# Optimization experiments

Hardware: AMD Instinct MI355X
Metric: run time of the kernel (lower is better)

The kernel has to match this reference:

```python
import jax, jax.numpy as jnp
import numpy as np

B, S, D = 2, 2048, 768
H = 12
HD = D // H  # 64
SCALE = HD ** -0.5


def setup_inputs() -> dict:
    key = jax.random.key(0)
    k1, k2, k3, k4, k5 = jax.random.split(key, 5)
    x = jax.random.normal(k1, (B, S, D), dtype=jnp.float32)
    w_qkv = jax.random.normal(k2, (D, 3 * D), dtype=jnp.float32) * (D ** -0.5)
    b_qkv = jax.random.normal(k3, (3 * D,), dtype=jnp.float32) * 0.02
    w_proj = jax.random.normal(k4, (D, D), dtype=jnp.float32) * (D ** -0.5)
    b_proj = jax.random.normal(k5, (D,), dtype=jnp.float32) * 0.02
    return {"x": x, "w_qkv": w_qkv, "b_qkv": b_qkv, "w_proj": w_proj, "b_proj": b_proj}


def reference(x, w_qkv, b_qkv, w_proj, b_proj):
    b, s, d = x.shape
    # QKV projection: (B,S,3D) -> (3,B,H,S,HD)
    qkv = x @ w_qkv + b_qkv
    qkv = qkv.reshape(b, s, 3, H, HD).transpose(2, 0, 3, 1, 4)
    q, k, v = qkv[0], qkv[1], qkv[2]
    q = q * SCALE
    # full NxN attention scores, as in the original module
    attn = jnp.einsum("bhqd,bhkd->bhqk", q, k)
    attn = jax.nn.softmax(attn, axis=-1)
    out = jnp.einsum("bhqk,bhkd->bhqd", attn, v)  # (B,H,S,HD)
    out = out.transpose(0, 2, 1, 3).reshape(b, s, d)
    return out @ w_proj + b_proj
```

## Files before the change

kernel.cpp:

```cpp
#include <hip/hip_runtime.h>
#include <hip/hip_bf16.h>

#define B_ 2
#define S_ 2048
#define D_ 768
#define H_ 12
#define HD_ 64
#define EXP2C_ 0.1803368801111244f

typedef __attribute__((ext_vector_type(8))) short bf16x8;
typedef __attribute__((ext_vector_type(8))) unsigned short u16x8;
typedef __attribute__((ext_vector_type(4))) float f32x4;

static __device__ __forceinline__ unsigned short f2bf(float x) {
    union { float f; unsigned u; } v; v.f = x;
    unsigned r = (v.u + 0x7FFFu + ((v.u >> 16) & 1u)) >> 16;
    return (unsigned short)r;
}
static __device__ __forceinline__ float bf2f(unsigned short h) {
    union { unsigned u; float f; } v; v.u = ((unsigned)h) << 16;
    return v.f;
}
static __device__ __forceinline__ float fexp2(float x) { return __builtin_exp2f(x); }

static __device__ __forceinline__ unsigned pk_bf16(float a, float b) {
    __hip_bfloat162 pk = __float22bfloat162_rn(make_float2(a, b));
    union { __hip_bfloat162 h; unsigned u; } v; v.h = pk;
    return v.u;
}

static __device__ __forceinline__ f32x4 mfma32(bf16x8 a, bf16x8 b, f32x4 c) {
    return __builtin_amdgcn_mfma_f32_16x16x32_bf16(a, b, c, 0, 0, 0);
}

typedef __attribute__((address_space(3))) unsigned int lds_u32;
typedef __attribute__((address_space(1))) const unsigned int glb_u32;
static __device__ __forceinline__ void glds16(const unsigned short* g, unsigned short* l) {
    __builtin_amdgcn_global_load_lds((glb_u32*)g, (lds_u32*)l, 16, 0, 0);
}

#define PREP_CONV_ 1536
#define PREP_TQKV_ 1728
#define PREP_TPRJ_ 576
__global__ __launch_bounds__(256) void prep_kernel(
    const float* __restrict__ x,      unsigned short* __restrict__ x16,
    const float* __restrict__ w_qkv,  unsigned short* __restrict__ wqkvT,
    const float* __restrict__ w_proj, unsigned short* __restrict__ wprojT)
{
    __shared__ float tile[32][33];
    const int bid = blockIdx.x, t = threadIdx.x;
    if (bid < PREP_CONV_) {
        const int i = (bid * 256 + t) * 8;
        float4 a0 = *(const float4*)(x + i);
        float4 a1 = *(const float4*)(x + i + 4);
        u16x8 s;
        s[0] = f2bf(a0.x); s[1] = f2bf(a0.y); s[2] = f2bf(a0.z); s[3] = f2bf(a0.w);
        s[4] = f2bf(a1.x); s[5] = f2bf(a1.y); s[6] = f2bf(a1.z); s[7] = f2bf(a1.w);
        *(u16x8*)(x16 + i) = s;
        return;
    }
    const float* w; unsigned short* wT; int N, bb;
    if (bid < PREP_CONV_ + PREP_TQKV_) { w = w_qkv; wT = wqkvT; N = 3 * D_; bb = bid - PREP_CONV_; }
    else                               { w = w_proj; wT = wprojT; N = D_;   bb = bid - PREP_CONV_ - PREP_TQKV_; }
    const int K = D_;
    const int nt = N / 32;
    const int n0 = (bb % nt) * 32, k0 = (bb / nt) * 32;
    const int tx = t & 31, ty = t >> 5;
#pragma unroll
    for (int i = 0; i < 4; i++)
        tile[ty + i * 8][tx] = w[(size_t)(k0 + ty + i * 8) * N + n0 + tx];
    __syncthreads();
#pragma unroll
    for (int i = 0; i < 4; i++)
        wT[(size_t)(n0 + ty + i * 8) * K + k0 + tx] = f2bf(tile[tx][ty + i * 8]);
}

template <int BM, int BN, bool OUT_F32>
__global__ __launch_bounds__(256) void gemm_bt_kernel(
    const unsigned short* __restrict__ A,
    const unsigned short* __restrict__ Bt,
    const float* __restrict__ bias,
    void* __restrict__ Cp,
    int M, int N, int K)
{
    __shared__ __align__(16) unsigned short As[BM][32];
    __shared__ __align__(16) unsigned short Bs[BN][32];
    constexpr int MI = BM / 32, NJ = BN / 32;
    constexpr int ACH = BM * 4, BCH = BN * 4;

    const int t = threadIdx.x;
    const int w = t >> 6, lane = t & 63, quad = lane >> 4, l16 = lane & 15;
    const int n0 = blockIdx.x * BN, m0 = blockIdx.y * BM;
    const int mw = (w & 1) * (BM / 2), nw = (w >> 1) * (BN / 2);

    const f32x4 z = {0.f, 0.f, 0.f, 0.f};
    f32x4 acc[MI][NJ];
#pragma unroll
    for (int i = 0; i < MI; i++)
#pragma unroll
        for (int j = 0; j < NJ; j++) acc[i][j] = z;

    for (int kk = 0; kk < K; kk += 32) {
#pragma unroll
        for (int it = 0; it < (ACH + 255) / 256; it++) {
            const int c = t + it * 256;
            if (ACH % 256 == 0 || c < ACH) {
                const int row = c >> 2, c8 = (c & 3) << 3;
                glds16(A + (size_t)(m0 + row) * K + kk + c8, &As[0][0] + c * 8);
            }
        }
#pragma unroll
        for (int it = 0; it < (BCH + 255) / 256; it++) {
            const int c = t + it * 256;
            if (BCH % 256 == 0 || c < BCH) {
                const int row = c >> 2, c8 = (c & 3) << 3;
                glds16(Bt + (size_t)(n0 + row) * K + kk + c8, &Bs[0][0] + c * 8);
            }
        }
        __syncthreads();

        bf16x8 a[MI], b[NJ];
#pragma unroll
        for (int i = 0; i < MI; i++)
            a[i] = *(const bf16x8*)(&As[mw + i * 16 + l16][quad * 8]);
#pragma unroll
        for (int j = 0; j < NJ; j++)
            b[j] = *(const bf16x8*)(&Bs[nw + j * 16 + l16][quad * 8]);
#pragma unroll
        for (int i = 0; i < MI; i++)
#pragma unroll
            for (int j = 0; j < NJ; j++)
                acc[i][j] = mfma32(a[i], b[j], acc[i][j]);
        __syncthreads();
    }

#pragma unroll
    for (int j = 0; j < NJ; j++) {
        const int col = n0 + nw + j * 16 + l16;
        const float bv = bias[col];
#pragma unroll
        for (int i = 0; i < MI; i++) {
#pragma unroll
            for (int r = 0; r < 4; r++) {
                const int row = m0 + mw + i * 16 + quad * 4 + r;
                const float v = acc[i][j][r] + bv;
                if (OUT_F32) ((float*)Cp)[(size_t)row * N + col] = v;
                else         ((unsigned short*)Cp)[(size_t)row * N + col] = f2bf(v);
            }
        }
    }
}

__global__ __launch_bounds__(256) void repack_v_kernel(
    const unsigned short* __restrict__ qkv,
    unsigned short* __restrict__ vt)
{
    __shared__ unsigned short T[64][65];
    const int t = threadIdx.x;
    const int bh = blockIdx.x, st = blockIdx.y;
    const int b = bh / H_, h = bh % H_;
    const unsigned short* src =
        qkv + (size_t)(b * S_ + st * 64) * (3 * D_) + 2 * D_ + h * HD_;

#pragma unroll
    for (int it = 0; it < 2; it++) {
        const int c = t + it * 256, sr = c >> 3, g = c & 7;
        u16x8 v = *(const u16x8*)(src + (size_t)sr * (3 * D_) + g * 8);
#pragma unroll
        for (int j = 0; j < 8; j++) T[sr][g * 8 + j] = v[j];
    }
    __syncthreads();
#pragma unroll
    for (int it = 0; it < 2; it++) {
        const int c = t + it * 256, hd = c >> 3, g = c & 7;
        u16x8 v;
#pragma unroll
        for (int j = 0; j < 8; j++) v[j] = T[g * 8 + j][hd];
        *(u16x8*)(vt + (size_t)(bh * HD_ + hd) * S_ + st * 64 + g * 8) = v;
    }
}

__global__ __launch_bounds__(256) void attn_kernel(
    const unsigned short* __restrict__ qkv,
    const unsigned short* __restrict__ vt,
    unsigned short* __restrict__ o)
{
    __shared__ __align__(16) unsigned short Ks[2][64][64];
    __shared__ __align__(16) unsigned short Vs[2][64][64];
    __shared__ __align__(16) unsigned short p_lds[4][16][64];

    const int t = threadIdx.x;
    const int w = t >> 6, lane = t & 63, quad = lane >> 4, l16 = lane & 15;
    const int h8 = l16 & 7;
    const int qt = blockIdx.x, bh = blockIdx.y;
    const int b = bh / H_, h = bh % H_;
    const int ld = 3 * D_;

    const unsigned short* qbase =
        qkv + (size_t)(b * S_ + qt * 64 + 16 * w + l16) * ld + h * HD_;
    u16x8 qr0 = *(const u16x8*)(qbase + quad * 8);
    u16x8 qr1 = *(const u16x8*)(qbase + 32 + quad * 8);
    bf16x8 qf0, qf1;
#pragma unroll
    for (int j = 0; j < 8; j++) {
        qf0[j] = (short)f2bf(bf2f(qr0[j]) * EXP2C_);
        qf1[j] = (short)f2bf(bf2f(qr1[j]) * EXP2C_);
    }

    const unsigned short* kbase = qkv + (size_t)(b * S_) * ld + D_ + h * HD_;
    const unsigned short* vbase = vt + (size_t)bh * HD_ * S_;

    const f32x4 z = {0.f, 0.f, 0.f, 0.f};
    f32x4 o_acc[4] = {z, z, z, z};
    f32x4 l4[4] = {z, z, z, z};

#pragma unroll
    for (int it = 0; it < 2; it++) {
        const int c = t + it * 256, row = c >> 3, g = c & 7, sg = g ^ (row & 7);
        *(u16x8*)(&Ks[0][row][sg * 8]) = *(const u16x8*)(kbase + (size_t)row * ld + g * 8);
        *(u16x8*)(&Vs[0][row][sg * 8]) = *(const u16x8*)(vbase + (size_t)row * S_ + g * 8);
    }
    __syncthreads();

    const int NT = S_ / 64;
    for (int kt = 0; kt < NT; kt++) {
        const int buf = kt & 1;
        const bool pre = (kt + 1 < NT);

        u16x8 pk[2], pv[2];
        if (pre) {
            const int kr1 = (kt + 1) * 64;
#pragma unroll
            for (int i = 0; i < 2; i++) {
                const int c = t + i * 256, row = c >> 3, g = c & 7;
                pk[i] = *(const u16x8*)(kbase + (size_t)(kr1 + row) * ld + g * 8);
                pv[i] = *(const u16x8*)(vbase + (size_t)row * S_ + kr1 + g * 8);
            }
        }

        f32x4 s_acc[4] = {z, z, z, z};
#pragma unroll
        for (int nt = 0; nt < 4; nt++) {
            const unsigned short* kr = &Ks[buf][nt * 16 + l16][0];
            bf16x8 k0 = *(const bf16x8*)(kr + (quad ^ h8) * 8);
            bf16x8 k1 = *(const bf16x8*)(kr + ((quad + 4) ^ h8) * 8);
            s_acc[nt] = mfma32(qf0, k0, s_acc[nt]);
            s_acc[nt] = mfma32(qf1, k1, s_acc[nt]);
        }

#pragma unroll
        for (int nt = 0; nt < 4; nt++) {
            f32x4 pv4;
#pragma unroll
            for (int r = 0; r < 4; r++) pv4[r] = fexp2(s_acc[nt][r]);
            l4[nt] += pv4;
            const unsigned u01 = pk_bf16(pv4[0], pv4[1]);
            const unsigned u23 = pk_bf16(pv4[2], pv4[3]);
            const int g = nt * 2 + (l16 >> 3), cw = l16 & 7;
#pragma unroll
            for (int r = 0; r < 4; r++) {
                const int row = quad * 4 + r;
                const unsigned short pv16 =
                    (r == 0) ? (unsigned short)u01 :
                    (r == 1) ? (unsigned short)(u01 >> 16) :
                    (r == 2) ? (unsigned short)u23 :
                               (unsigned short)(u23 >> 16);
                p_lds[w][row][(g ^ (row & 7)) * 8 + cw] = pv16;
            }
        }
        bf16x8 pa0 = *(const bf16x8*)(&p_lds[w][l16][(quad ^ h8) * 8]);
        bf16x8 pa1 = *(const bf16x8*)(&p_lds[w][l16][((quad + 4) ^ h8) * 8]);

#pragma unroll
        for (int nt = 0; nt < 4; nt++) {
            const int row = nt * 16 + l16;
            bf16x8 v0 = *(const bf16x8*)(&Vs[buf][row][(quad ^ h8) * 8]);
            bf16x8 v1 = *(const bf16x8*)(&Vs[buf][row][((quad + 4) ^ h8) * 8]);
            o_acc[nt] = mfma32(pa0, v0, o_acc[nt]);
            o_acc[nt] = mfma32(pa1, v1, o_acc[nt]);
        }

        if (pre) {
#pragma unroll
            for (int i = 0; i < 2; i++) {
                const int c = t + i * 256, row = c >> 3, g = c & 7, sg = g ^ (row & 7);
                *(u16x8*)(&Ks[buf ^ 1][row][sg * 8]) = pk[i];
                *(u16x8*)(&Vs[buf ^ 1][row][sg * 8]) = pv[i];
            }
        }
        __syncthreads();
    }

#pragma unroll
    for (int r = 0; r < 4; r++) {
        float l = l4[0][r] + l4[1][r] + l4[2][r] + l4[3][r];
        l += __shfl_xor(l, 1, 64); l += __shfl_xor(l, 2, 64);
        l += __shfl_xor(l, 4, 64); l += __shfl_xor(l, 8, 64);
        const float inv = 1.f / l;
        const int row = b * S_ + qt * 64 + 16 * w + quad * 4 + r;
        unsigned short* ob = o + (size_t)row * D_ + h * HD_;
#pragma unroll
        for (int nt = 0; nt < 4; nt++)
            ob[nt * 16 + l16] = f2bf(o_acc[nt][r] * inv);
    }
}

extern "C" void kernel_launch(void* const* d_in, const int* in_sizes, int n_in,
                              void* d_out, int out_size, void* d_ws, size_t ws_size,
                              hipStream_t stream) {
    const float* x      = (const float*)d_in[0];
    const float* w_qkv  = (const float*)d_in[1];
    const float* b_qkv  = (const float*)d_in[2];
    const float* w_proj = (const float*)d_in[3];
    const float* b_proj = (const float*)d_in[4];
    float* out = (float*)d_out;

    unsigned short* qkv    = (unsigned short*)d_ws;
    unsigned short* vtb    = qkv    + (size_t)(B_ * S_) * (3 * D_);
    unsigned short* o_x16  = vtb    + (size_t)(B_ * H_) * HD_ * S_;
    unsigned short* wqkvT  = o_x16  + (size_t)(B_ * S_) * D_;
    unsigned short* wprojT = wqkvT  + (size_t)D_ * (3 * D_);

    dim3 blk(256);
    prep_kernel<<<dim3(PREP_CONV_ + PREP_TQKV_ + PREP_TPRJ_), blk, 0, stream>>>(
        x, o_x16, w_qkv, wqkvT, w_proj, wprojT);
    gemm_bt_kernel<128, 96, false><<<dim3((3 * D_) / 96, (B_ * S_) / 128), blk, 0, stream>>>(
        o_x16, wqkvT, b_qkv, qkv, B_ * S_, 3 * D_, D_);
    repack_v_kernel<<<dim3(B_ * H_, S_ / 64), blk, 0, stream>>>(qkv, vtb);
    attn_kernel<<<dim3(S_ / 64, B_ * H_), blk, 0, stream>>>(qkv, vtb, o_x16);
    gemm_bt_kernel<64, 64, true><<<dim3(D_ / 64, (B_ * S_) / 64), blk, 0, stream>>>(
        o_x16, wprojT, b_proj, out, B_ * S_, D_, D_);
}
```

Before: 176.7 us.

## Compute transposed S tile so P stays in registers, dropping LDS round-trip

Swaps the MFMA operands for the QK^T product so each lane holds a column of scores in the layout the PV MFMA needs as its A operand, with K rows permuted and a new swizzle for the K shared-memory tile. This removes the per-iteration P write/read through LDS and its per-element 16-bit stores. The row-sum reduction is reworked for the transposed layout, using cross-quad shuffles and a broadcast per output row. The risk is correctness of the row permutation and swizzle mapping.

```diff
diff --git a/kernel.cpp b/kernel.cpp
--- a/kernel.cpp
+++ b/kernel.cpp
@@ -11,6 +11,7 @@
 typedef __attribute__((ext_vector_type(8))) short bf16x8;
 typedef __attribute__((ext_vector_type(8))) unsigned short u16x8;
 typedef __attribute__((ext_vector_type(4))) float f32x4;
+typedef __attribute__((ext_vector_type(4))) unsigned int u32x4;
 
 static __device__ __forceinline__ unsigned short f2bf(float x) {
     union { float f; unsigned u; } v; v.f = x;
@@ -187,7 +188,6 @@
 {
     __shared__ __align__(16) unsigned short Ks[2][64][64];
     __shared__ __align__(16) unsigned short Vs[2][64][64];
-    __shared__ __align__(16) unsigned short p_lds[4][16][64];
 
     const int t = threadIdx.x;
     const int w = t >> 6, lane = t & 63, quad = lane >> 4, l16 = lane & 15;
@@ -216,9 +216,11 @@
 
 #pragma unroll
     for (int it = 0; it < 2; it++) {
-        const int c = t + it * 256, row = c >> 3, g = c & 7, sg = g ^ (row & 7);
-        *(u16x8*)(&Ks[0][row][sg * 8]) = *(const u16x8*)(kbase + (size_t)row * ld + g * 8);
-        *(u16x8*)(&Vs[0][row][sg * 8]) = *(const u16x8*)(vbase + (size_t)row * S_ + g * 8);
+        const int c = t + it * 256, row = c >> 3, g = c & 7;
+        const int sgK = g ^ ((row & 3) | (((row >> 3) & 1) << 2));
+        const int sgV = g ^ (row & 7);
+        *(u16x8*)(&Ks[0][row][sgK * 8]) = *(const u16x8*)(kbase + (size_t)row * ld + g * 8);
+        *(u16x8*)(&Vs[0][row][sgV * 8]) = *(const u16x8*)(vbase + (size_t)row * S_ + g * 8);
     }
     __syncthreads();
 
@@ -241,35 +243,32 @@
         f32x4 s_acc[4] = {z, z, z, z};
 #pragma unroll
         for (int nt = 0; nt < 4; nt++) {
-            const unsigned short* kr = &Ks[buf][nt * 16 + l16][0];
-            bf16x8 k0 = *(const bf16x8*)(kr + (quad ^ h8) * 8);
-            bf16x8 k1 = *(const bf16x8*)(kr + ((quad + 4) ^ h8) * 8);
-            s_acc[nt] = mfma32(qf0, k0, s_acc[nt]);
-            s_acc[nt] = mfma32(qf1, k1, s_acc[nt]);
-        }
-
+            const int rowp = ((nt >> 1) << 5) + ((l16 >> 2) << 3) + ((nt & 1) << 2) + (l16 & 3);
+            const int skr = (rowp & 3) | (((rowp >> 3) & 1) << 2);
+            const unsigned short* kr = &Ks[buf][rowp][0];
+            bf16x8 k0 = *(const bf16x8*)(kr + (quad ^ skr) * 8);
+            bf16x8 k1 = *(const bf16x8*)(kr + ((quad ^ skr) ^ 4) * 8);
+            s_acc[nt] = mfma32(k0, qf0, s_acc[nt]);
+            s_acc[nt] = mfma32(k1, qf1, s_acc[nt]);
+        }
+
+        f32x4 pr[4];
 #pragma unroll
         for (int nt = 0; nt < 4; nt++) {
-            f32x4 pv4;
-#pragma unroll
-            for (int r = 0; r < 4; r++) pv4[r] = fexp2(s_acc[nt][r]);
-            l4[nt] += pv4;
-            const unsigned u01 = pk_bf16(pv4[0], pv4[1]);
-            const unsigned u23 = pk_bf16(pv4[2], pv4[3]);
-            const int g = nt * 2 + (l16 >> 3), cw = l16 & 7;
-#pragma unroll
-            for (int r = 0; r < 4; r++) {
-                const int row = quad * 4 + r;
-                const unsigned short pv16 =
-                    (r == 0) ? (unsigned short)u01 :
-                    (r == 1) ? (unsigned short)(u01 >> 16) :
-                    (r == 2) ? (unsigned short)u23 :
-                               (unsigned short)(u23 >> 16);
-                p_lds[w][row][(g ^ (row & 7)) * 8 + cw] = pv16;
-            }
-        }
-        bf16x8 pa0 = *(const bf16x8*)(&p_lds[w][l16][(quad ^ h8) * 8]);
-        bf16x8 pa1 = *(const bf16x8*)(&p_lds[w][l16][((quad + 4) ^ h8) * 8]);
+#pragma unroll
+            for (int r = 0; r < 4; r++) pr[nt][r] = fexp2(s_acc[nt][r]);
+            l4[nt] += pr[nt];
+        }
+        union { u32x4 u; bf16x8 h; } ca, cb;
+        ca.u[0] = pk_bf16(pr[0][0], pr[0][1]);
+        ca.u[1] = pk_bf16(pr[0][2], pr[0][3]);
+        ca.u[2] = pk_bf16(pr[1][0], pr[1][1]);
+        ca.u[3] = pk_bf16(pr[1][2], pr[1][3]);
+        cb.u[0] = pk_bf16(pr[2][0], pr[2][1]);
+        cb.u[1] = pk_bf16(pr[2][2], pr[2][3]);
+        cb.u[2] = pk_bf16(pr[3][0], pr[3][1]);
+        cb.u[3] = pk_bf16(pr[3][2], pr[3][3]);
+        const bf16x8 pa0 = ca.h, pa1 = cb.h;
 
 #pragma unroll
         for (int nt = 0; nt < 4; nt++) {
@@ -283,20 +282,26 @@
         if (pre) {
 #pragma unroll
             for (int i = 0; i < 2; i++) {
-                const int c = t + i * 256, row = c >> 3, g = c & 7, sg = g ^ (row & 7);
-                *(u16x8*)(&Ks[buf ^ 1][row][sg * 8]) = pk[i];
-                *(u16x8*)(&Vs[buf ^ 1][row][sg * 8]) = pv[i];
+                const int c = t + i * 256, row = c >> 3, g = c & 7;
+                const int sgK = g ^ ((row & 3) | (((row >> 3) & 1) << 2));
+                const int sgV = g ^ (row & 7);
+                *(u16x8*)(&Ks[buf ^ 1][row][sgK * 8]) = pk[i];
+                *(u16x8*)(&Vs[buf ^ 1][row][sgV * 8]) = pv[i];
             }
         }
         __syncthreads();
     }
 
+    float l = 0.f;
+#pragma unroll
+    for (int nt = 0; nt < 4; nt++)
+        l += l4[nt][0] + l4[nt][1] + l4[nt][2] + l4[nt][3];
+    l += __shfl_xor(l, 16, 64);
+    l += __shfl_xor(l, 32, 64);
 #pragma unroll
     for (int r = 0; r < 4; r++) {
-        float l = l4[0][r] + l4[1][r] + l4[2][r] + l4[3][r];
-        l += __shfl_xor(l, 1, 64); l += __shfl_xor(l, 2, 64);
-        l += __shfl_xor(l, 4, 64); l += __shfl_xor(l, 8, 64);
-        const float inv = 1.f / l;
+        const float lr = __shfl(l, quad * 4 + r, 64);
+        const float inv = 1.f / lr;
         const int row = b * S_ + qt * 64 + 16 * w + quad * 4 + r;
         unsigned short* ob = o + (size_t)row * D_ + h * HD_;
 #pragma unroll
```

Result: no change. 173.5 us (-1.8%).
